# Kernel optimization log

Measured on AMD Instinct MI355X. Metric: run time of the kernel, lower is better.

The kernel has to match this reference:

```python
import jax, jax.numpy as jnp
import numpy as np

NEG_SLOPE = 0.2


def _gat_conv(x, src, dst, W, a_src, a_dst, b, n_nodes):
    # Single-head PyG GATConv (normalize arg in source is ignored by GATConv).
    h = x @ W                                   # [N, C_out]
    e_src = h @ a_src                           # [N] alpha_src contribution
    e_dst = h @ a_dst                           # [N] alpha_dst contribution
    logits = jax.nn.leaky_relu(e_src[src] + e_dst[dst], NEG_SLOPE)  # [E]
    m = jax.ops.segment_max(logits, dst, num_segments=n_nodes)      # per-dst max
    e = jnp.exp(logits - m[dst])
    denom = jax.ops.segment_sum(e, dst, num_segments=n_nodes)
    alpha = e / denom[dst]                      # edge softmax over in-neighbors
    out = jax.ops.segment_sum(h[src] * alpha[:, None], dst, num_segments=n_nodes)
    return out + b


def _add_self_loops(edge_index, n_nodes):
    loop = jnp.arange(n_nodes, dtype=edge_index.dtype)
    src = jnp.concatenate([edge_index[0], loop])
    dst = jnp.concatenate([edge_index[1], loop])
    return src, dst


def setup_inputs() -> dict:
    key = jax.random.key(0)
    ks = jax.random.split(key, 16)
    N, E, C_IN, C_HID, C_OUT = 50000, 1600000, 128, 128, 64
    x = jax.random.normal(ks[0], (N, C_IN), dtype=jnp.float32)
    edge_index = jax.random.randint(ks[1], (2, E), 0, N, dtype=jnp.int32)
    glorot = lambda k, shape: jax.random.normal(k, shape, jnp.float32) * np.sqrt(2.0 / sum(shape))
    return {
        "x": x,
        "edge_index": edge_index,
        "W0": glorot(ks[2], (C_IN, C_HID)),
        "as0": glorot(ks[3], (C_HID,)) * 0.1,
        "ad0": glorot(ks[4], (C_HID,)) * 0.1,
        "b0": jnp.zeros((C_HID,), jnp.float32),
        "W1": glorot(ks[5], (C_HID, C_HID)),
        "as1": glorot(ks[6], (C_HID,)) * 0.1,
        "ad1": glorot(ks[7], (C_HID,)) * 0.1,
        "b1": jnp.zeros((C_HID,), jnp.float32),
        "W2": glorot(ks[8], (C_HID, C_OUT)),
        "as2": glorot(ks[9], (C_OUT,)) * 0.1,
        "ad2": glorot(ks[10], (C_OUT,)) * 0.1,
        "b2": jnp.zeros((C_OUT,), jnp.float32),
    }


def reference(x, edge_index, W0, as0, ad0, b0, W1, as1, ad1, b1, W2, as2, ad2, b2):
    n_nodes = x.shape[0]
    src, dst = _add_self_loops(edge_index, n_nodes)
    # eval mode: F.dropout with training=False is identity
    h = jax.nn.relu(_gat_conv(x, src, dst, W0, as0, ad0, b0, n_nodes))
    h = jax.nn.relu(_gat_conv(h, src, dst, W1, as1, ad1, b1, n_nodes))
    out = _gat_conv(h, src, dst, W2, as2, ad2, b2, n_nodes)
    return out
```

## Files before the change

### kernel.cpp

```cpp
#include <hip/hip_runtime.h>
#include <hip/hip_bf16.h>
#include <type_traits>

#define DEVFN __device__ __forceinline__

typedef __attribute__((ext_vector_type(8))) short bfrag;
typedef __attribute__((ext_vector_type(4))) float facc4;

DEVFN float lrelu(float v) { return (v >= 0.f) ? v : 0.2f * v; }

DEVFN float2 bf2x2(unsigned u) {
  return make_float2(__uint_as_float(u << 16), __uint_as_float(u & 0xFFFF0000u));
}
DEVFN float bf1(unsigned short b) { return __uint_as_float(((unsigned)b) << 16); }
DEVFN unsigned short f2bf(float f) {
  __hip_bfloat16 h = __float2bfloat16(f);
  return *reinterpret_cast<unsigned short*>(&h);
}
DEVFN unsigned packbf2(float x, float y) {
  return (unsigned)f2bf(x) | ((unsigned)f2bf(y) << 16);
}

DEVFN float wave_sum(float v) {
#pragma unroll
  for (int o = 1; o < 64; o <<= 1) v += __shfl_xor(v, o, 64);
  return v;
}
DEVFN float wave_max(float v) {
#pragma unroll
  for (int o = 1; o < 64; o <<= 1) v = fmaxf(v, __shfl_xor(v, o, 64));
  return v;
}

template<int C, bool A_FP32>
__global__ __launch_bounds__(256) void gemm_mfma(const void* __restrict__ Xin,
                                                 const float* __restrict__ W,
                                                 const float* __restrict__ a_src,
                                                 const float* __restrict__ a_dst,
                                                 unsigned short* __restrict__ H,
                                                 float* __restrict__ es,
                                                 float* __restrict__ ed,
                                                 int N) {
  constexpr int K = 128;
  constexpr int LSTR = K + 8;
  constexpr int NT = C / 16;
  __shared__ unsigned short WsT[C * LSTR];

  const int t = threadIdx.x;
  for (int i = t; i < K * C; i += 256) {
    int k = i / C;
    int c = i - k * C;
    WsT[c * LSTR + k] = f2bf(W[i]);
  }
  __syncthreads();

  const int wave = t >> 6;
  const int lane = t & 63;
  const int l15 = lane & 15;
  const int quad = lane >> 4;
  const int arow = blockIdx.x * 64 + wave * 16 + l15;
  const bool avalid = arow < N;

  facc4 acc[NT];
#pragma unroll
  for (int i = 0; i < NT; ++i) acc[i] = (facc4){0.f, 0.f, 0.f, 0.f};

#pragma unroll
  for (int ks = 0; ks < 4; ++ks) {
    bfrag a;
    if (A_FP32) {
      if (avalid) {
        const float* xp = (const float*)Xin + (size_t)arow * K + quad * 8 + ks * 32;
        float4 u = *(const float4*)xp;
        float4 v = *(const float4*)(xp + 4);
        a[0] = (short)f2bf(u.x); a[1] = (short)f2bf(u.y);
        a[2] = (short)f2bf(u.z); a[3] = (short)f2bf(u.w);
        a[4] = (short)f2bf(v.x); a[5] = (short)f2bf(v.y);
        a[6] = (short)f2bf(v.z); a[7] = (short)f2bf(v.w);
      } else {
        a = (bfrag){0, 0, 0, 0, 0, 0, 0, 0};
      }
    } else {
      const unsigned short* xp =
          (const unsigned short*)Xin + (size_t)arow * K + quad * 8 + ks * 32;
      a = *(const bfrag*)xp;
    }
#pragma unroll
    for (int ct = 0; ct < NT; ++ct) {
      bfrag b = *(const bfrag*)(&WsT[(ct * 16 + l15) * LSTR + ks * 32 + quad * 8]);
      acc[ct] = __builtin_amdgcn_mfma_f32_16x16x32_bf16(a, b, acc[ct], 0, 0, 0);
    }
  }

  float asv[NT], adv[NT];
#pragma unroll
  for (int ct = 0; ct < NT; ++ct) {
    asv[ct] = a_src[ct * 16 + l15];
    adv[ct] = a_dst[ct * 16 + l15];
  }

  const int orow0 = blockIdx.x * 64 + wave * 16 + quad * 4;
#pragma unroll
  for (int r = 0; r < 4; ++r) {
    const int orow = orow0 + r;
    float ps = 0.f, pd = 0.f;
#pragma unroll
    for (int ct = 0; ct < NT; ++ct) {
      if (orow < N) H[(size_t)orow * C + ct * 16 + l15] = f2bf(acc[ct][r]);
      ps += acc[ct][r] * asv[ct];
      pd += acc[ct][r] * adv[ct];
    }
#pragma unroll
    for (int msk = 1; msk < 16; msk <<= 1) {
      ps += __shfl_xor(ps, msk, 64);
      pd += __shfl_xor(pd, msk, 64);
    }
    if (l15 == 0 && orow < N) { es[orow] = ps; ed[orow] = pd; }
  }
}

__global__ void hist_only(const int* __restrict__ dst, int* __restrict__ hmat,
                          int E, int nbk, int chunk) {
  __shared__ int hist[4 * 128];
  const int t = threadIdx.x;
  for (int i = t; i < 4 * 128; i += 256) hist[i] = 0;
  __syncthreads();
  int* h = &hist[(t >> 6) << 7];
  const int e0 = blockIdx.x * chunk;
  const int e1 = min(E, e0 + chunk);
  for (int e = e0 + t; e < e1; e += 256) {
    atomicAdd(&h[dst[e] >> 9], 1);
  }
  __syncthreads();
  if (t < nbk)
    hmat[t * gridDim.x + blockIdx.x] =
        hist[t] + hist[t + 128] + hist[t + 256] + hist[t + 384];
}

__global__ void scan_partial(const int* __restrict__ in, int* __restrict__ csum, int n) {
  __shared__ int sh[256];
  int i = blockIdx.x * 256 + threadIdx.x;
  sh[threadIdx.x] = (i < n) ? in[i] : 0;
  __syncthreads();
  for (int o = 128; o > 0; o >>= 1) {
    if (threadIdx.x < o) sh[threadIdx.x] += sh[threadIdx.x + o];
    __syncthreads();
  }
  if (threadIdx.x == 0) csum[blockIdx.x] = sh[0];
}

__global__ void scan_chunks(int* __restrict__ csum, int nch) {
  __shared__ int sh[256];
  __shared__ int carry;
  if (threadIdx.x == 0) carry = 0;
  __syncthreads();
  for (int base = 0; base < nch; base += 256) {
    int i = base + threadIdx.x;
    int v = (i < nch) ? csum[i] : 0;
    sh[threadIdx.x] = v;
    __syncthreads();
    for (int o = 1; o < 256; o <<= 1) {
      int t = (threadIdx.x >= o) ? sh[threadIdx.x - o] : 0;
      __syncthreads();
      sh[threadIdx.x] += t;
      __syncthreads();
    }
    if (i < nch) csum[i] = carry + sh[threadIdx.x] - v;
    __syncthreads();
    if (threadIdx.x == 255) carry += sh[255];
    __syncthreads();
  }
}

__global__ void scan_final(const int* __restrict__ deg, const int* __restrict__ csum,
                           int* __restrict__ rp, int* __restrict__ wp, int N, int E) {
  __shared__ int sh[256];
  int i = blockIdx.x * 256 + threadIdx.x;
  int v = (i < N) ? deg[i] : 0;
  sh[threadIdx.x] = v;
  __syncthreads();
  for (int o = 1; o < 256; o <<= 1) {
    int t = (threadIdx.x >= o) ? sh[threadIdx.x - o] : 0;
    __syncthreads();
    sh[threadIdx.x] += t;
    __syncthreads();
  }
  if (i < N) {
    int r = csum[blockIdx.x] + sh[threadIdx.x] - v;
    rp[i] = r;
    wp[i] = r;
  }
  if (blockIdx.x == 0 && threadIdx.x == 0) rp[N] = E;
}

__global__ void scan_final_excl(const int* __restrict__ in, const int* __restrict__ csum,
                                int* __restrict__ out, int n) {
  __shared__ int sh[256];
  int i = blockIdx.x * 256 + threadIdx.x;
  int v = (i < n) ? in[i] : 0;
  sh[threadIdx.x] = v;
  __syncthreads();
  for (int o = 1; o < 256; o <<= 1) {
    int t = (threadIdx.x >= o) ? sh[threadIdx.x - o] : 0;
    __syncthreads();
    sh[threadIdx.x] += t;
    __syncthreads();
  }
  if (i < n) out[i] = csum[blockIdx.x] + sh[threadIdx.x] - v;
}

__global__ void place_pass(const int* __restrict__ src, const int* __restrict__ dst,
                           const int* __restrict__ off, int2* __restrict__ be,
                           int E, int nbk, int chunk) {
  __shared__ int cur[128];
  const int t = threadIdx.x;
  if (t < nbk) cur[t] = off[t * gridDim.x + blockIdx.x];
  __syncthreads();
  const int e0 = blockIdx.x * chunk;
  const int e1 = min(E, e0 + chunk);
  for (int e = e0 + t; e < e1; e += 256) {
    int d = dst[e];
    int s = src[e];
    int p = atomicAdd(&cur[d >> 9], 1);
    be[p] = make_int2(s, d);
  }
}

__global__ void bucket_final(const int2* __restrict__ be, const int* __restrict__ off,
                             int* __restrict__ rp, unsigned short* __restrict__ col,
                             int E, int N, int nbk, int pblk) {
  __shared__ int cur[512];
  __shared__ int ps[256];
  const int b = blockIdx.x;
  const int n0 = b << 9;
  const int cnt = min(512, N - n0);
  const int t = threadIdx.x;
  for (int i = t; i < cnt; i += 256) cur[i] = 0;
  __syncthreads();
  const int e0 = off[b * pblk];
  const int e1 = (b + 1 < nbk) ? off[(b + 1) * pblk] : E;
  for (int e = e0 + t; e < e1; e += 256) {
    int2 sd = be[e];
    atomicAdd(&cur[sd.y - n0], 1);
  }
  __syncthreads();
  const int i0 = 2 * t, i1 = 2 * t + 1;
  const int v0 = (i0 < cnt) ? cur[i0] : 0;
  const int v1 = (i1 < cnt) ? cur[i1] : 0;
  ps[t] = v0 + v1;
  __syncthreads();
  for (int o = 1; o < 256; o <<= 1) {
    int u = (t >= o) ? ps[t - o] : 0;
    __syncthreads();
    ps[t] += u;
    __syncthreads();
  }
  const int base = e0 + ps[t] - (v0 + v1);
  if (i0 < cnt) { rp[n0 + i0] = base;      cur[i0] = base; }
  if (i1 < cnt) { rp[n0 + i1] = base + v0; cur[i1] = base + v0; }
  if (b == nbk - 1 && t == 0) rp[N] = E;
  __syncthreads();
  for (int e = e0 + t; e < e1; e += 256) {
    int2 sd = be[e];
    int p = atomicAdd(&cur[sd.y - n0], 1);
    col[p] = (unsigned short)sd.x;
  }
}

__global__ void csr_scatter_ranged(const int* __restrict__ src,
                                   const int* __restrict__ dst,
                                   int* __restrict__ wp, int* __restrict__ col,
                                   int E, int range, int npass) {
  const int stride = gridDim.x * blockDim.x;
  const int gid = blockIdx.x * blockDim.x + threadIdx.x;
  for (int pass = 0; pass < npass; ++pass) {
    const int lo = pass * range;
    const int hi = lo + range;
    for (int e = gid; e < E; e += stride) {
      int d = dst[e];
      if (d >= lo && d < hi) {
        int p = atomicAdd(wp + d, 1);
        col[p] = src[e];
      }
    }
  }
}

__global__ void csr_count(const int* __restrict__ dst, int* __restrict__ deg, int E) {
  int e = blockIdx.x * blockDim.x + threadIdx.x;
  if (e < E) atomicAdd(deg + dst[e], 1);
}

template<bool RELU, bool OUT_BF16, typename IT>
__global__ void gat_fused128(const int* __restrict__ row_ptr,
                             const IT* __restrict__ col,
                             const float* __restrict__ es,
                             const float* __restrict__ ed,
                             const unsigned short* __restrict__ H,
                             const float* __restrict__ bias,
                             void* __restrict__ outX, int N) {
  const int lane = threadIdx.x & 63;
  const int n = blockIdx.x * (blockDim.x >> 6) + (threadIdx.x >> 6);
  if (n >= N) return;

  const int k0 = row_ptr[n];
  const int k1 = row_ptr[n + 1];
  const int deg = k1 - k0;
  const float edd = ed[n];
  const float self_lg = lrelu(es[n] + edd);

  const unsigned* Hp = (const unsigned*)H;
  float ax0 = 0.f, ay0 = 0.f, ax1 = 0.f, ay1 = 0.f;
  float den, sp;

  if (deg <= 64) {
    int k = k0 + lane;
    bool act = (k < k1);
    int c = act ? (int)col[k] : 0;
    float lg = act ? lrelu(es[c] + edd) : -3.0e38f;
    float m = fmaxf(wave_max(lg), self_lg);
    float p = act ? __expf(lg - m) : 0.f;
    sp = __expf(self_lg - m);
    den = wave_sum(p) + sp;
    int j = 0;
    for (; j + 8 <= deg; j += 8) {
      int ss[8];
      float pp[8];
      unsigned uu[8];
#pragma unroll
      for (int q = 0; q < 8; ++q) {
        ss[q] = __shfl(c, j + q);
        pp[q] = __shfl(p, j + q);
      }
#pragma unroll
      for (int q = 0; q < 8; ++q) uu[q] = Hp[(size_t)ss[q] * 64 + lane];
#pragma unroll
      for (int q = 0; q < 8; ++q) {
        float2 h = bf2x2(uu[q]);
        if (q & 1) { ax1 += pp[q] * h.x; ay1 += pp[q] * h.y; }
        else       { ax0 += pp[q] * h.x; ay0 += pp[q] * h.y; }
      }
    }
    for (; j < deg; ++j) {
      int s = __shfl(c, j);
      float pj = __shfl(p, j);
      float2 h = bf2x2(Hp[(size_t)s * 64 + lane]);
      ax0 += pj * h.x; ay0 += pj * h.y;
    }
  } else {
    float mloc = self_lg;
    for (int base = k0; base < k1; base += 64) {
      int k = base + lane;
      if (k < k1) mloc = fmaxf(mloc, lrelu(es[(int)col[k]] + edd));
    }
    float m = wave_max(mloc);
    sp = __expf(self_lg - m);
    den = sp;
    for (int base = k0; base < k1; base += 64) {
      int k = base + lane;
      bool act = (k < k1);
      int c = act ? (int)col[k] : 0;
      float p = act ? __expf(lrelu(es[c] + edd) - m) : 0.f;
      den += wave_sum(p);
      int len = min(64, k1 - base);
      for (int j = 0; j < len; ++j) {
        int s = __shfl(c, j);
        float pj = __shfl(p, j);
        float2 h = bf2x2(Hp[(size_t)s * 64 + lane]);
        ax0 += pj * h.x; ay0 += pj * h.y;
      }
    }
  }

  float2 hv = bf2x2(Hp[(size_t)n * 64 + lane]);
  ax0 += sp * hv.x; ay0 += sp * hv.y;
  float inv = 1.f / den;
  float2 bv = ((const float2*)bias)[lane];
  float vx = (ax0 + ax1) * inv + bv.x;
  float vy = (ay0 + ay1) * inv + bv.y;
  if (RELU) { vx = fmaxf(vx, 0.f); vy = fmaxf(vy, 0.f); }
  if (OUT_BF16)
    ((unsigned*)outX)[(size_t)n * 64 + lane] = packbf2(vx, vy);
  else
    ((float2*)outX)[(size_t)n * 64 + lane] = make_float2(vx, vy);
}

template<bool RELU, typename IT>
__global__ void gat_fused64(const int* __restrict__ row_ptr,
                            const IT* __restrict__ col,
                            const float* __restrict__ es,
                            const float* __restrict__ ed,
                            const unsigned short* __restrict__ H,
                            const float* __restrict__ bias,
                            float* __restrict__ outX, int N) {
  const int lane = threadIdx.x & 63;
  const int n = blockIdx.x * (blockDim.x >> 6) + (threadIdx.x >> 6);
  if (n >= N) return;

  const int k0 = row_ptr[n];
  const int k1 = row_ptr[n + 1];
  const int deg = k1 - k0;
  const float edd = ed[n];
  const float self_lg = lrelu(es[n] + edd);

  float a0 = 0.f, a1 = 0.f;
  float den, sp;

  if (deg <= 64) {
    int k = k0 + lane;
    bool act = (k < k1);
    int c = act ? (int)col[k] : 0;
    float lg = act ? lrelu(es[c] + edd) : -3.0e38f;
    float m = fmaxf(wave_max(lg), self_lg);
    float p = act ? __expf(lg - m) : 0.f;
    sp = __expf(self_lg - m);
    den = wave_sum(p) + sp;
    int j = 0;
    for (; j + 8 <= deg; j += 8) {
      int ss[8];
      float pp[8];
      unsigned short uu[8];
#pragma unroll
      for (int q = 0; q < 8; ++q) {
        ss[q] = __shfl(c, j + q);
        pp[q] = __shfl(p, j + q);
      }
#pragma unroll
      for (int q = 0; q < 8; ++q) uu[q] = H[(size_t)ss[q] * 64 + lane];
#pragma unroll
      for (int q = 0; q < 8; ++q) {
        if (q & 1) a1 += pp[q] * bf1(uu[q]);
        else       a0 += pp[q] * bf1(uu[q]);
      }
    }
    for (; j < deg; ++j) {
      int s = __shfl(c, j);
      float pj = __shfl(p, j);
      a0 += pj * bf1(H[(size_t)s * 64 + lane]);
    }
  } else {
    float mloc = self_lg;
    for (int base = k0; base < k1; base += 64) {
      int k = base + lane;
      if (k < k1) mloc = fmaxf(mloc, lrelu(es[(int)col[k]] + edd));
    }
    float m = wave_max(mloc);
    sp = __expf(self_lg - m);
    den = sp;
    for (int base = k0; base < k1; base += 64) {
      int k = base + lane;
      bool act = (k < k1);
      int c = act ? (int)col[k] : 0;
      float p = act ? __expf(lrelu(es[c] + edd) - m) : 0.f;
      den += wave_sum(p);
      int len = min(64, k1 - base);
      for (int j = 0; j < len; ++j) {
        int s = __shfl(c, j);
        float pj = __shfl(p, j);
        a0 += pj * bf1(H[(size_t)s * 64 + lane]);
      }
    }
  }

  a0 += sp * bf1(H[(size_t)n * 64 + lane]);
  float v = (a0 + a1) / den + bias[lane];
  if (RELU) v = fmaxf(v, 0.f);
  outX[(size_t)n * 64 + lane] = v;
}


extern "C" void kernel_launch(void* const* d_in, const int* in_sizes, int n_in,
                              void* d_out, int out_size, void* d_ws, size_t ws_size,
                              hipStream_t stream) {
  const int C_HID = in_sizes[3];
  const int C_FIN = in_sizes[11];
  const int C_IN  = in_sizes[2] / C_HID;
  const int N     = in_sizes[0] / C_IN;
  const int E     = in_sizes[1] / 2;
  const int NPAD  = ((N + 63) / 64) * 64;

  const float* x = (const float*)d_in[0];
  const int* ei  = (const int*)d_in[1];
  const int* src = ei;
  const int* dst = ei + E;

  const float* W0  = (const float*)d_in[2];
  const float* as0 = (const float*)d_in[3];
  const float* ad0 = (const float*)d_in[4];
  const float* b0  = (const float*)d_in[5];
  const float* W1  = (const float*)d_in[6];
  const float* as1 = (const float*)d_in[7];
  const float* ad1 = (const float*)d_in[8];
  const float* b1  = (const float*)d_in[9];
  const float* W2  = (const float*)d_in[10];
  const float* as2 = (const float*)d_in[11];
  const float* ad2 = (const float*)d_in[12];
  const float* b2  = (const float*)d_in[13];

  char* base = (char*)d_ws;
  size_t off = 0;
  auto alloc = [&](size_t bytes) -> char* {
    char* p = base + off;
    off = (off + bytes + 255) & ~((size_t)255);
    return p;
  };
  const int PBLK = 512;
  const int NBK  = (N + 511) >> 9;
  const int M    = NBK * PBLK;
  const int NCH  = (N + 255) / 256;
  const int MCH  = (M + 255) / 256;
  const int SCH  = (NCH > MCH ? NCH : MCH);

  unsigned short* XB  = (unsigned short*)alloc((size_t)NPAD * C_HID * 2);
  unsigned short* H   = (unsigned short*)alloc((size_t)N * C_HID * 2);
  float* ES    = (float*)alloc((size_t)N * sizeof(float));
  float* ED    = (float*)alloc((size_t)N * sizeof(float));
  int*   RP    = (int*)alloc((size_t)(N + 1) * sizeof(int));
  int*   WP    = (int*)alloc((size_t)N * sizeof(int));
  void*  COL   = (void*)alloc((size_t)E * sizeof(int));
  int*   DEG   = (int*)alloc((size_t)N * sizeof(int));
  int*   CSUM  = (int*)alloc((size_t)SCH * sizeof(int));
  int*   HMAT  = (int*)alloc((size_t)M * sizeof(int));
  int*   OFF   = (int*)alloc((size_t)M * sizeof(int));
  int2*  BE    = (int2*)alloc((size_t)E * sizeof(int2));
  (void)ws_size;

  const int wgrid = (N + 3) / 4;
  const int mgrid = NPAD / 64;
  const bool u16 = (N <= 65535);

  if (u16) {
    const int CHUNK = (E + PBLK - 1) / PBLK;
    hist_only<<<PBLK, 256, 0, stream>>>(dst, HMAT, E, NBK, CHUNK);
    scan_partial<<<MCH, 256, 0, stream>>>(HMAT, CSUM, M);
    scan_chunks<<<1, 256, 0, stream>>>(CSUM, MCH);
    scan_final_excl<<<MCH, 256, 0, stream>>>(HMAT, CSUM, OFF, M);
    place_pass<<<PBLK, 256, 0, stream>>>(src, dst, OFF, BE, E, NBK, CHUNK);
    bucket_final<<<NBK, 256, 0, stream>>>(BE, OFF, RP, (unsigned short*)COL,
                                          E, N, NBK, PBLK);
  } else {
    hipMemsetAsync(DEG, 0, (size_t)N * sizeof(int), stream);
    const int ET256 = (E + 255) / 256;
    csr_count<<<ET256, 256, 0, stream>>>(dst, DEG, E);
    scan_partial<<<NCH, 256, 0, stream>>>(DEG, CSUM, N);
    scan_chunks<<<1, 256, 0, stream>>>(CSUM, NCH);
    scan_final<<<NCH, 256, 0, stream>>>(DEG, CSUM, RP, WP, N, E);
    const int NPASS = 8;
    const int range = (N + NPASS - 1) / NPASS;
    csr_scatter_ranged<<<2048, 256, 0, stream>>>(src, dst, WP, (int*)COL, E,
                                                 range, NPASS);
  }

  auto run_layers = [&](auto* col) {
    using IT = typename std::remove_pointer<decltype(col)>::type;
    gemm_mfma<128, true><<<mgrid, 256, 0, stream>>>(x, W0, as0, ad0, H, ES, ED, N);
    gat_fused128<true, true, IT><<<wgrid, 256, 0, stream>>>(RP, col, ES, ED, H, b0, XB, N);
    gemm_mfma<128, false><<<mgrid, 256, 0, stream>>>(XB, W1, as1, ad1, H, ES, ED, N);
    gat_fused128<true, true, IT><<<wgrid, 256, 0, stream>>>(RP, col, ES, ED, H, b1, XB, N);
    gemm_mfma<64, false><<<mgrid, 256, 0, stream>>>(XB, W2, as2, ad2, H, ES, ED, N);
    gat_fused64<false, IT><<<wgrid, 256, 0, stream>>>(RP, col, ES, ED, H, b2,
                                                      (float*)d_out, N);
  };

  if (u16) run_layers((unsigned short*)COL);
  else     run_layers((int*)COL);
  (void)out_size; (void)n_in;
}
```

Measured before the change: 346.7 us.

## Gather multiple neighbor rows per wave with 16-byte vector loads in GAT aggregation

The aggregation kernels now split each wave into sub-groups. Each sub-group reads a whole neighbor feature row with 16-byte uint4 loads, so one wave processes several edges at once instead of one edge per iteration with 4- or 2-byte loads. The partial sums are combined with cross-lane xor-shuffle reductions, and only the first sub-group writes the output with vector stores. This cuts the number of dependent gather iterations and memory instructions per edge. In exchange it adds reduction shuffles, and lanes past the degree read clamped indices whose weight p is zero, which is wasted load work on low-degree nodes.

```diff
diff --git a/kernel.cpp b/kernel.cpp
--- a/kernel.cpp
+++ b/kernel.cpp
@@ -12,7 +12,8 @@
 DEVFN float2 bf2x2(unsigned u) {
   return make_float2(__uint_as_float(u << 16), __uint_as_float(u & 0xFFFF0000u));
 }
-DEVFN float bf1(unsigned short b) { return __uint_as_float(((unsigned)b) << 16); }
+DEVFN float bf_lo(unsigned u) { return __uint_as_float(u << 16); }
+DEVFN float bf_hi(unsigned u) { return __uint_as_float(u & 0xFFFF0000u); }
 DEVFN unsigned short f2bf(float f) {
   __hip_bfloat16 h = __float2bfloat16(f);
   return *reinterpret_cast<unsigned short*>(&h);
@@ -291,7 +292,7 @@
   if (e < E) atomicAdd(deg + dst[e], 1);
 }
 
-template<bool RELU, bool OUT_BF16, typename IT>
+template<bool RELU, typename IT>
 __global__ void gat_fused128(const int* __restrict__ row_ptr,
                              const IT* __restrict__ col,
                              const float* __restrict__ es,
@@ -303,14 +304,19 @@
   const int n = blockIdx.x * (blockDim.x >> 6) + (threadIdx.x >> 6);
   if (n >= N) return;
 
+  const int g4 = lane >> 4;
+  const int l15 = lane & 15;
+
   const int k0 = row_ptr[n];
   const int k1 = row_ptr[n + 1];
   const int deg = k1 - k0;
   const float edd = ed[n];
   const float self_lg = lrelu(es[n] + edd);
 
-  const unsigned* Hp = (const unsigned*)H;
-  float ax0 = 0.f, ay0 = 0.f, ax1 = 0.f, ay1 = 0.f;
+  const char* Hb = (const char*)H;
+  float acc[8];
+#pragma unroll
+  for (int i = 0; i < 8; ++i) acc[i] = 0.f;
   float den, sp;
 
   if (deg <= 64) {
@@ -322,30 +328,23 @@
     float p = act ? __expf(lg - m) : 0.f;
     sp = __expf(self_lg - m);
     den = wave_sum(p) + sp;
-    int j = 0;
-    for (; j + 8 <= deg; j += 8) {
-      int ss[8];
-      float pp[8];
-      unsigned uu[8];
-#pragma unroll
-      for (int q = 0; q < 8; ++q) {
-        ss[q] = __shfl(c, j + q);
-        pp[q] = __shfl(p, j + q);
-      }
-#pragma unroll
-      for (int q = 0; q < 8; ++q) uu[q] = Hp[(size_t)ss[q] * 64 + lane];
-#pragma unroll
-      for (int q = 0; q < 8; ++q) {
-        float2 h = bf2x2(uu[q]);
-        if (q & 1) { ax1 += pp[q] * h.x; ay1 += pp[q] * h.y; }
-        else       { ax0 += pp[q] * h.x; ay0 += pp[q] * h.y; }
-      }
-    }
-    for (; j < deg; ++j) {
-      int s = __shfl(c, j);
-      float pj = __shfl(p, j);
-      float2 h = bf2x2(Hp[(size_t)s * 64 + lane]);
-      ax0 += pj * h.x; ay0 += pj * h.y;
+    for (int j = 0; j < deg; j += 8) {
+      int i0 = min(j + g4, 63);
+      int i1 = min(j + 4 + g4, 63);
+      int c0 = __shfl(c, i0);
+      int c1 = __shfl(c, i1);
+      float p0 = __shfl(p, i0);
+      float p1 = __shfl(p, i1);
+      uint4 v0 = *(const uint4*)(Hb + (((size_t)c0 << 8) + l15 * 16));
+      uint4 v1 = *(const uint4*)(Hb + (((size_t)c1 << 8) + l15 * 16));
+      acc[0] += p0 * bf_lo(v0.x); acc[1] += p0 * bf_hi(v0.x);
+      acc[2] += p0 * bf_lo(v0.y); acc[3] += p0 * bf_hi(v0.y);
+      acc[4] += p0 * bf_lo(v0.z); acc[5] += p0 * bf_hi(v0.z);
+      acc[6] += p0 * bf_lo(v0.w); acc[7] += p0 * bf_hi(v0.w);
+      acc[0] += p1 * bf_lo(v1.x); acc[1] += p1 * bf_hi(v1.x);
+      acc[2] += p1 * bf_lo(v1.y); acc[3] += p1 * bf_hi(v1.y);
+      acc[4] += p1 * bf_lo(v1.z); acc[5] += p1 * bf_hi(v1.z);
+      acc[6] += p1 * bf_lo(v1.w); acc[7] += p1 * bf_hi(v1.w);
     }
   } else {
     float mloc = self_lg;
@@ -363,26 +362,57 @@
       float p = act ? __expf(lrelu(es[c] + edd) - m) : 0.f;
       den += wave_sum(p);
       int len = min(64, k1 - base);
-      for (int j = 0; j < len; ++j) {
-        int s = __shfl(c, j);
-        float pj = __shfl(p, j);
-        float2 h = bf2x2(Hp[(size_t)s * 64 + lane]);
-        ax0 += pj * h.x; ay0 += pj * h.y;
+      for (int j = 0; j < len; j += 8) {
+        int i0 = min(j + g4, 63);
+        int i1 = min(j + 4 + g4, 63);
+        int c0 = __shfl(c, i0);
+        int c1 = __shfl(c, i1);
+        float p0 = __shfl(p, i0);
+        float p1 = __shfl(p, i1);
+        uint4 v0 = *(const uint4*)(Hb + (((size_t)c0 << 8) + l15 * 16));
+        uint4 v1 = *(const uint4*)(Hb + (((size_t)c1 << 8) + l15 * 16));
+        acc[0] += p0 * bf_lo(v0.x); acc[1] += p0 * bf_hi(v0.x);
+        acc[2] += p0 * bf_lo(v0.y); acc[3] += p0 * bf_hi(v0.y);
+        acc[4] += p0 * bf_lo(v0.z); acc[5] += p0 * bf_hi(v0.z);
+        acc[6] += p0 * bf_lo(v0.w); acc[7] += p0 * bf_hi(v0.w);
+        acc[0] += p1 * bf_lo(v1.x); acc[1] += p1 * bf_hi(v1.x);
+        acc[2] += p1 * bf_lo(v1.y); acc[3] += p1 * bf_hi(v1.y);
+        acc[4] += p1 * bf_lo(v1.z); acc[5] += p1 * bf_hi(v1.z);
+        acc[6] += p1 * bf_lo(v1.w); acc[7] += p1 * bf_hi(v1.w);
       }
     }
   }
 
-  float2 hv = bf2x2(Hp[(size_t)n * 64 + lane]);
-  ax0 += sp * hv.x; ay0 += sp * hv.y;
+#pragma unroll
+  for (int i = 0; i < 8; ++i) {
+    acc[i] += __shfl_xor(acc[i], 16, 64);
+    acc[i] += __shfl_xor(acc[i], 32, 64);
+  }
+
+  uint4 hv = *(const uint4*)(Hb + (((size_t)n << 8) + l15 * 16));
+  acc[0] += sp * bf_lo(hv.x); acc[1] += sp * bf_hi(hv.x);
+  acc[2] += sp * bf_lo(hv.y); acc[3] += sp * bf_hi(hv.y);
+  acc[4] += sp * bf_lo(hv.z); acc[5] += sp * bf_hi(hv.z);
+  acc[6] += sp * bf_lo(hv.w); acc[7] += sp * bf_hi(hv.w);
+
   float inv = 1.f / den;
-  float2 bv = ((const float2*)bias)[lane];
-  float vx = (ax0 + ax1) * inv + bv.x;
-  float vy = (ay0 + ay1) * inv + bv.y;
-  if (RELU) { vx = fmaxf(vx, 0.f); vy = fmaxf(vy, 0.f); }
-  if (OUT_BF16)
-    ((unsigned*)outX)[(size_t)n * 64 + lane] = packbf2(vx, vy);
-  else
-    ((float2*)outX)[(size_t)n * 64 + lane] = make_float2(vx, vy);
+  float4 bv0 = *(const float4*)(bias + l15 * 8);
+  float4 bv1 = *(const float4*)(bias + l15 * 8 + 4);
+  float o0 = acc[0] * inv + bv0.x, o1 = acc[1] * inv + bv0.y;
+  float o2 = acc[2] * inv + bv0.z, o3 = acc[3] * inv + bv0.w;
+  float o4 = acc[4] * inv + bv1.x, o5 = acc[5] * inv + bv1.y;
+  float o6 = acc[6] * inv + bv1.z, o7 = acc[7] * inv + bv1.w;
+  if (RELU) {
+    o0 = fmaxf(o0, 0.f); o1 = fmaxf(o1, 0.f); o2 = fmaxf(o2, 0.f);
+    o3 = fmaxf(o3, 0.f); o4 = fmaxf(o4, 0.f); o5 = fmaxf(o5, 0.f);
+    o6 = fmaxf(o6, 0.f); o7 = fmaxf(o7, 0.f);
+  }
+  if (g4 == 0) {
+    uint4 w;
+    w.x = packbf2(o0, o1); w.y = packbf2(o2, o3);
+    w.z = packbf2(o4, o5); w.w = packbf2(o6, o7);
+    *(uint4*)((char*)outX + (((size_t)n << 8) + l15 * 16)) = w;
+  }
 }
 
 template<bool RELU, typename IT>
@@ -397,13 +427,19 @@
   const int n = blockIdx.x * (blockDim.x >> 6) + (threadIdx.x >> 6);
   if (n >= N) return;
 
+  const int g8 = lane >> 3;
+  const int l8 = lane & 7;
+
   const int k0 = row_ptr[n];
   const int k1 = row_ptr[n + 1];
   const int deg = k1 - k0;
   const float edd = ed[n];
   const float self_lg = lrelu(es[n] + edd);
 
-  float a0 = 0.f, a1 = 0.f;
+  const char* Hb = (const char*)H;
+  float acc[8];
+#pragma unroll
+  for (int i = 0; i < 8; ++i) acc[i] = 0.f;
   float den, sp;
 
   if (deg <= 64) {
@@ -415,28 +451,15 @@
     float p = act ? __expf(lg - m) : 0.f;
     sp = __expf(self_lg - m);
     den = wave_sum(p) + sp;
-    int j = 0;
-    for (; j + 8 <= deg; j += 8) {
-      int ss[8];
-      float pp[8];
-      unsigned short uu[8];
-#pragma unroll
-      for (int q = 0; q < 8; ++q) {
-        ss[q] = __shfl(c, j + q);
-        pp[q] = __shfl(p, j + q);
-      }
-#pragma unroll
-      for (int q = 0; q < 8; ++q) uu[q] = H[(size_t)ss[q] * 64 + lane];
-#pragma unroll
-      for (int q = 0; q < 8; ++q) {
-        if (q & 1) a1 += pp[q] * bf1(uu[q]);
-        else       a0 += pp[q] * bf1(uu[q]);
-      }
-    }
-    for (; j < deg; ++j) {
-      int s = __shfl(c, j);
-      float pj = __shfl(p, j);
-      a0 += pj * bf1(H[(size_t)s * 64 + lane]);
+    for (int j = 0; j < deg; j += 8) {
+      int i0 = min(j + g8, 63);
+      int c0 = __shfl(c, i0);
+      float p0 = __shfl(p, i0);
+      uint4 v0 = *(const uint4*)(Hb + (((size_t)c0 << 7) + l8 * 16));
+      acc[0] += p0 * bf_lo(v0.x); acc[1] += p0 * bf_hi(v0.x);
+      acc[2] += p0 * bf_lo(v0.y); acc[3] += p0 * bf_hi(v0.y);
+      acc[4] += p0 * bf_lo(v0.z); acc[5] += p0 * bf_hi(v0.z);
+      acc[6] += p0 * bf_lo(v0.w); acc[7] += p0 * bf_hi(v0.w);
     }
   } else {
     float mloc = self_lg;
@@ -454,18 +477,51 @@
       float p = act ? __expf(lrelu(es[c] + edd) - m) : 0.f;
       den += wave_sum(p);
       int len = min(64, k1 - base);
-      for (int j = 0; j < len; ++j) {
-        int s = __shfl(c, j);
-        float pj = __shfl(p, j);
-        a0 += pj * bf1(H[(size_t)s * 64 + lane]);
+      for (int j = 0; j < len; j += 8) {
+        int i0 = min(j + g8, 63);
+        int c0 = __shfl(c, i0);
+        float p0 = __shfl(p, i0);
+        uint4 v0 = *(const uint4*)(Hb + (((size_t)c0 << 7) + l8 * 16));
+        acc[0] += p0 * bf_lo(v0.x); acc[1] += p0 * bf_hi(v0.x);
+        acc[2] += p0 * bf_lo(v0.y); acc[3] += p0 * bf_hi(v0.y);
+        acc[4] += p0 * bf_lo(v0.z); acc[5] += p0 * bf_hi(v0.z);
+        acc[6] += p0 * bf_lo(v0.w); acc[7] += p0 * bf_hi(v0.w);
       }
     }
   }
 
-  a0 += sp * bf1(H[(size_t)n * 64 + lane]);
-  float v = (a0 + a1) / den + bias[lane];
-  if (RELU) v = fmaxf(v, 0.f);
-  outX[(size_t)n * 64 + lane] = v;
+#pragma unroll
+  for (int i = 0; i < 8; ++i) {
+    acc[i] += __shfl_xor(acc[i], 8, 64);
+    acc[i] += __shfl_xor(acc[i], 16, 64);
+    acc[i] += __shfl_xor(acc[i], 32, 64);
+  }
+
+  uint4 hv = *(const uint4*)(Hb + (((size_t)n << 7) + l8 * 16));
+  acc[0] += sp * bf_lo(hv.x); acc[1] += sp * bf_hi(hv.x);
+  acc[2] += sp * bf_lo(hv.y); acc[3] += sp * bf_hi(hv.y);
+  acc[4] += sp * bf_lo(hv.z); acc[5] += sp * bf_hi(hv.z);
+  acc[6] += sp * bf_lo(hv.w); acc[7] += sp * bf_hi(hv.w);
+
+  float inv = 1.f / den;
+  float4 bv0 = *(const float4*)(bias + l8 * 8);
+  float4 bv1 = *(const float4*)(bias + l8 * 8 + 4);
+  float4 w0, w1;
+  w0.x = acc[0] * inv + bv0.x; w0.y = acc[1] * inv + bv0.y;
+  w0.z = acc[2] * inv + bv0.z; w0.w = acc[3] * inv + bv0.w;
+  w1.x = acc[4] * inv + bv1.x; w1.y = acc[5] * inv + bv1.y;
+  w1.z = acc[6] * inv + bv1.z; w1.w = acc[7] * inv + bv1.w;
+  if (RELU) {
+    w0.x = fmaxf(w0.x, 0.f); w0.y = fmaxf(w0.y, 0.f);
+    w0.z = fmaxf(w0.z, 0.f); w0.w = fmaxf(w0.w, 0.f);
+    w1.x = fmaxf(w1.x, 0.f); w1.y = fmaxf(w1.y, 0.f);
+    w1.z = fmaxf(w1.z, 0.f); w1.w = fmaxf(w1.w, 0.f);
+  }
+  if (g8 == 0) {
+    char* op = (char*)outX + (((size_t)n << 8) + l8 * 32);
+    *(float4*)op = w0;
+    *(float4*)(op + 16) = w1;
+  }
 }
 
 
@@ -554,9 +610,9 @@
   auto run_layers = [&](auto* col) {
     using IT = typename std::remove_pointer<decltype(col)>::type;
     gemm_mfma<128, true><<<mgrid, 256, 0, stream>>>(x, W0, as0, ad0, H, ES, ED, N);
-    gat_fused128<true, true, IT><<<wgrid, 256, 0, stream>>>(RP, col, ES, ED, H, b0, XB, N);
+    gat_fused128<true, IT><<<wgrid, 256, 0, stream>>>(RP, col, ES, ED, H, b0, XB, N);
     gemm_mfma<128, false><<<mgrid, 256, 0, stream>>>(XB, W1, as1, ad1, H, ES, ED, N);
-    gat_fused128<true, true, IT><<<wgrid, 256, 0, stream>>>(RP, col, ES, ED, H, b1, XB, N);
+    gat_fused128<true, IT><<<wgrid, 256, 0, stream>>>(RP, col, ES, ED, H, b1, XB, N);
     gemm_mfma<64, false><<<mgrid, 256, 0, stream>>>(XB, W2, as2, ad2, H, ES, ED, N);
     gat_fused64<false, IT><<<wgrid, 256, 0, stream>>>(RP, col, ES, ED, H, b2,
                                                       (float*)d_out, N);
```

Result: faster. 332.2 us (-4.2%).
